# Optimization experiments

Measured on AMD Instinct MI355X. Metric: run time of the kernel, lower is better.

The kernel has to match this reference:

```python
import jax, jax.numpy as jnp
import numpy as np


def setup_inputs() -> dict:
    key = jax.random.key(0)
    k1, k2 = jax.random.split(key)
    B, T, D = 32, 1024, 768
    x = jax.random.normal(k1, (B, T, D), dtype=jnp.float32)
    # integer frame durations per token; int(d + 0.5) == d for non-negative ints,
    # so this matches the torch module's rounding exactly
    dur = jax.random.randint(k2, (B, T), 0, 8).astype(jnp.int32)
    return {"x": x, "dur": dur}


def reference(x, dur):
    """Duration-based repeat-interleave per batch row, zero-padded to the batch max length.

    x:   [B, T, D] float frames
    dur: [B, T]    int   per-frame repeat counts (torch: int(dur + 0.5))
    returns [B, max_len, D] where max_len = max_b sum_t dur[b, t]
    """
    B, T, D = x.shape
    lens = dur  # already integral; torch's int(d + 0.5) is identity here
    totals = jnp.sum(lens, axis=1)  # [B]
    # torch pads to the batch-dependent max expanded length; materialize it as a
    # static Python int (dur is a concrete input, not traced here)
    max_len = int(jax.device_get(jnp.max(totals)))

    def expand_one(xb, lb):
        # cumulative end offsets of each source frame in the expanded sequence
        cs = jnp.cumsum(lb)                                   # [T]
        t = jnp.arange(max_len)                               # [max_len]
        # output frame t comes from the first source i with cs[i] > t
        src = jnp.searchsorted(cs, t, side='right')           # [max_len]
        src = jnp.minimum(src, T - 1)                         # clamp for padded tail
        out = jnp.take(xb, src, axis=0)                       # [max_len, D] gather
        valid = (t < cs[-1]).astype(xb.dtype)[:, None]        # zero-pad beyond total
        return out * valid

    return jax.vmap(expand_one)(x, lens)
```

## Files before the change

kernel.cpp:

```cpp
#include <hip/hip_runtime.h>

#define BATCH 32

typedef float f32x4 __attribute__((ext_vector_type(4)));
typedef int   i32x4 __attribute__((ext_vector_type(4)));

__global__ void lr_fused_kernel(const float* __restrict__ x,
                                const int* __restrict__ dur,
                                float* __restrict__ out,
                                int T, int D, int max_len) {
    const int b = blockIdx.y;
    const int tid = threadIdx.y * 64 + threadIdx.x;
    const int lane = tid & 63;
    const int w = tid >> 6;

    __shared__ int cs[1024];
    __shared__ int part[4];

    const i32x4* __restrict__ drow = reinterpret_cast<const i32x4*>(dur + b * T);
    const i32x4 d = drow[tid];
    const int s0 = d.x;
    const int s1 = s0 + d.y;
    const int s2 = s1 + d.z;
    const int s3 = s2 + d.w;

    int v = s3;
    #pragma unroll
    for (int off = 1; off < 64; off <<= 1) {
        int u = __shfl_up(v, off, 64);
        if (lane >= off) v += u;
    }
    if (lane == 63) part[w] = v;
    __syncthreads();

    int add = 0;
    if (w > 0) add += part[0];
    if (w > 1) add += part[1];
    if (w > 2) add += part[2];

    const int base = add + v - s3;
    cs[tid * 4 + 0] = base + s0;
    cs[tid * 4 + 1] = base + s1;
    cs[tid * 4 + 2] = base + s2;
    cs[tid * 4 + 3] = base + s3;
    __syncthreads();

    const int r = blockIdx.x * 4 + w;
    const int d4 = D >> 2;
    const int total = cs[T - 1];

    if (r < T) {
        const int end = cs[r];
        const int start = (r == 0) ? 0 : cs[r - 1];
        if (start != end) {
            const f32x4* __restrict__ sp =
                reinterpret_cast<const f32x4*>(x + ((size_t)b * T + r) * D);
            const f32x4 v0 = __builtin_nontemporal_load(&sp[lane]);
            const f32x4 v1 = __builtin_nontemporal_load(&sp[lane + 64]);
            const f32x4 v2 = __builtin_nontemporal_load(&sp[lane + 128]);

            f32x4* __restrict__ dst =
                reinterpret_cast<f32x4*>(out + ((size_t)b * max_len + start) * D);
            for (int j = start; j < end; ++j) {
                __builtin_nontemporal_store(v0, &dst[lane]);
                __builtin_nontemporal_store(v1, &dst[lane + 64]);
                __builtin_nontemporal_store(v2, &dst[lane + 128]);
                dst += d4;
            }
        }

        const f32x4 z = (f32x4)(0.f);
        for (int t = total + r; t < max_len; t += T) {
            f32x4* __restrict__ zp =
                reinterpret_cast<f32x4*>(out + ((size_t)b * max_len + t) * D);
            __builtin_nontemporal_store(z, &zp[lane]);
            __builtin_nontemporal_store(z, &zp[lane + 64]);
            __builtin_nontemporal_store(z, &zp[lane + 128]);
        }
    }
}

extern "C" void kernel_launch(void* const* d_in, const int* in_sizes, int n_in,
                              void* d_out, int out_size, void* d_ws, size_t ws_size,
                              hipStream_t stream) {
    const float* x = (const float*)d_in[0];
    const int* dur = (const int*)d_in[1];
    float* out = (float*)d_out;

    const int BT = in_sizes[1];
    const int B = BATCH;
    const int T = BT / B;
    const int D = in_sizes[0] / BT;
    const int max_len = out_size / (B * D);

    dim3 block(64, 4);
    dim3 grid((T + 3) / 4, B);
    lr_fused_kernel<<<grid, block, 0, stream>>>(x, dur, out, T, D, max_len);
}
```

Measured before the change: 94.83 us.

## Process four source frames per wave with prefetch of next frame

Each wave now handles four consecutive source frames instead of one, and the grid shrinks fourfold. Loading the next frame's data before storing the current one's repeats is meant to overlap load latency with stores. It also cuts the number of blocks that recompute the per-row duration prefix scan, and adds launch bounds for occupancy. The cost is less parallelism and more registers per thread. The code also assumes T is divisible by 16 and drops the r<T guard.

```diff
diff --git a/kernel.cpp b/kernel.cpp
--- a/kernel.cpp
+++ b/kernel.cpp
@@ -1,15 +1,18 @@
 #include <hip/hip_runtime.h>
 
 #define BATCH 32
+#define FPW 4
 
 typedef float f32x4 __attribute__((ext_vector_type(4)));
 typedef int   i32x4 __attribute__((ext_vector_type(4)));
 
-__global__ void lr_fused_kernel(const float* __restrict__ x,
-                                const int* __restrict__ dur,
-                                float* __restrict__ out,
-                                int T, int D, int max_len) {
+__global__ __launch_bounds__(256, 8)
+void lr_stream_kernel(const float* __restrict__ x,
+                      const int* __restrict__ dur,
+                      float* __restrict__ out,
+                      int T, int D, int max_len) {
     const int b = blockIdx.y;
+    const int bx = blockIdx.x;
     const int tid = threadIdx.y * 64 + threadIdx.x;
     const int lane = tid & 63;
     const int w = tid >> 6;
@@ -17,8 +20,7 @@
     __shared__ int cs[1024];
     __shared__ int part[4];
 
-    const i32x4* __restrict__ drow = reinterpret_cast<const i32x4*>(dur + b * T);
-    const i32x4 d = drow[tid];
+    const i32x4 d = reinterpret_cast<const i32x4*>(dur + b * T)[tid];
     const int s0 = d.x;
     const int s1 = s0 + d.y;
     const int s2 = s1 + d.z;
@@ -45,38 +47,53 @@
     cs[tid * 4 + 3] = base + s3;
     __syncthreads();
 
-    const int r = blockIdx.x * 4 + w;
+    const int total = cs[T - 1];
     const int d4 = D >> 2;
-    const int total = cs[T - 1];
 
-    if (r < T) {
-        const int end = cs[r];
-        const int start = (r == 0) ? 0 : cs[r - 1];
-        if (start != end) {
-            const f32x4* __restrict__ sp =
-                reinterpret_cast<const f32x4*>(x + ((size_t)b * T + r) * D);
-            const f32x4 v0 = __builtin_nontemporal_load(&sp[lane]);
-            const f32x4 v1 = __builtin_nontemporal_load(&sp[lane + 64]);
-            const f32x4 v2 = __builtin_nontemporal_load(&sp[lane + 128]);
+    const int fbase = (bx * 4 + w) * FPW;
+    int st[FPW + 1];
+    st[0] = (fbase == 0) ? 0 : cs[fbase - 1];
+    #pragma unroll
+    for (int k = 0; k < FPW; ++k) st[k + 1] = cs[fbase + k];
 
-            f32x4* __restrict__ dst =
-                reinterpret_cast<f32x4*>(out + ((size_t)b * max_len + start) * D);
-            for (int j = start; j < end; ++j) {
-                __builtin_nontemporal_store(v0, &dst[lane]);
-                __builtin_nontemporal_store(v1, &dst[lane + 64]);
-                __builtin_nontemporal_store(v2, &dst[lane + 128]);
-                dst += d4;
-            }
+    const f32x4* __restrict__ xb =
+        reinterpret_cast<const f32x4*>(x + (size_t)b * T * D);
+
+    f32x4 a0, a1, a2, n0, n1, n2;
+    if (st[1] > st[0]) {
+        const f32x4* sp = xb + (size_t)fbase * d4;
+        a0 = __builtin_nontemporal_load(&sp[lane]);
+        a1 = __builtin_nontemporal_load(&sp[lane + 64]);
+        a2 = __builtin_nontemporal_load(&sp[lane + 128]);
+    }
+    #pragma unroll
+    for (int k = 0; k < FPW; ++k) {
+        if (k + 1 < FPW && st[k + 2] > st[k + 1]) {
+            const f32x4* sp = xb + (size_t)(fbase + k + 1) * d4;
+            n0 = __builtin_nontemporal_load(&sp[lane]);
+            n1 = __builtin_nontemporal_load(&sp[lane + 64]);
+            n2 = __builtin_nontemporal_load(&sp[lane + 128]);
         }
+        f32x4* __restrict__ dst =
+            reinterpret_cast<f32x4*>(out + ((size_t)b * max_len + st[k]) * D);
+        for (int j = st[k]; j < st[k + 1]; ++j) {
+            __builtin_nontemporal_store(a0, &dst[lane]);
+            __builtin_nontemporal_store(a1, &dst[lane + 64]);
+            __builtin_nontemporal_store(a2, &dst[lane + 128]);
+            dst += d4;
+        }
+        a0 = n0; a1 = n1; a2 = n2;
+    }
 
-        const f32x4 z = (f32x4)(0.f);
-        for (int t = total + r; t < max_len; t += T) {
-            f32x4* __restrict__ zp =
-                reinterpret_cast<f32x4*>(out + ((size_t)b * max_len + t) * D);
-            __builtin_nontemporal_store(z, &zp[lane]);
-            __builtin_nontemporal_store(z, &zp[lane + 64]);
-            __builtin_nontemporal_store(z, &zp[lane + 128]);
-        }
+    const int q = bx * 4 + w;
+    const int nq = (T / (4 * FPW)) * 4;
+    const f32x4 z = (f32x4)(0.f);
+    for (int t = total + q; t < max_len; t += nq) {
+        f32x4* __restrict__ zp =
+            reinterpret_cast<f32x4*>(out + ((size_t)b * max_len + t) * D);
+        __builtin_nontemporal_store(z, &zp[lane]);
+        __builtin_nontemporal_store(z, &zp[lane + 64]);
+        __builtin_nontemporal_store(z, &zp[lane + 128]);
     }
 }
 
@@ -94,6 +111,6 @@
     const int max_len = out_size / (B * D);
 
     dim3 block(64, 4);
-    dim3 grid((T + 3) / 4, B);
-    lr_fused_kernel<<<grid, block, 0, stream>>>(x, dur, out, T, D, max_len);
+    dim3 grid(T / (4 * FPW), B);
+    lr_stream_kernel<<<grid, block, 0, stream>>>(x, dur, out, T, D, max_len);
 }
```

New measurement: 94.65 us. About the same (-0.2%).
